# Kernel tuning notes

Measured on AMD Instinct MI355X. Metric: run time of the kernel, lower is better.

## Reference

```python
import jax, jax.numpy as jnp
import numpy as np
import math

N, M, DIM = 16384, 4096, 1024


def setup_inputs() -> dict:
    key = jax.random.key(0)
    k1, k2, k3, k4, k5 = jax.random.split(key, 5)
    x = jax.random.normal(k1, (N, DIM), dtype=jnp.float32)
    e_repr = jax.random.normal(k2, (M, DIM), dtype=jnp.float32)
    H = jax.random.randint(k3, (N, M), 0, 2, dtype=jnp.int32)  # incidence matrix, >0 = connected
    # nn.Linear(dim, dim, bias=False) weights, scaled like torch default init
    W_e = jax.random.normal(k4, (DIM, DIM), dtype=jnp.float32) / math.sqrt(DIM)
    W_n = jax.random.normal(k5, (DIM, DIM), dtype=jnp.float32) / math.sqrt(DIM)
    return {"x": x, "e_repr": e_repr, "H": H, "W_e": W_e, "W_n": W_n}


def reference(x, e_repr, H, W_e, W_n):
    he = e_repr @ W_e.T            # [M, dim]  (W_e(e_repr); original recomputes this, same math)
    hn = x @ W_n.T                 # [N, dim]
    scale = 1.0 / math.sqrt(he.shape[1])
    B = (hn @ he.T) * scale        # [N, M] scores
    mask = H > 0
    B = jnp.where(mask, B, -1e9)
    B = jax.nn.softmax(B, axis=1) * mask.astype(B.dtype)
    out = jax.nn.elu(B @ he)       # [N, dim]
    return out, B
```

## Files before the change

kernel.cpp:

```cpp
#include <hip/hip_runtime.h>

#define NN 16384
#define MM 4096
#define DD 1024

typedef unsigned short u16;
typedef unsigned int u32;
typedef short bf16x8 __attribute__((ext_vector_type(8)));
typedef float f32x4 __attribute__((ext_vector_type(4)));

enum { EPI_PLAIN = 0, EPI_MASK = 1, EPI_ELU = 2 };

__global__ void sentinel_kernel(float* out, float val) {
    if (blockIdx.x == 0 && threadIdx.x < 64) out[threadIdx.x] = val;
}

template <int EPI>
__global__ __launch_bounds__(256) void gemm_split(
    const float* __restrict__ A, const float* __restrict__ Bt,
    float* __restrict__ C, const int* __restrict__ Hm,
    int Cc, int K)
{
    __shared__ u16 sAh[128][40];
    __shared__ u16 sAl[128][40];
    __shared__ u16 sBh[128][40];
    __shared__ u16 sBl[128][40];

    const int tid = threadIdx.x;
    const int lane = tid & 63;
    const int w = tid >> 6;
    const int wm = (w >> 1) * 64;
    const int wn = (w & 1) * 64;
    const int l15 = lane & 15;
    const int l4 = lane >> 4;
    const int rowBlk = blockIdx.y * 128;
    const int colBlk = blockIdx.x * 128;
    const int sr = tid >> 1;
    const int sk = (tid & 1) * 16;

    f32x4 acc[4][4] = {};

    union V16 { u16 u[16]; bf16x8 v[2]; };

    for (int k0 = 0; k0 < K; k0 += 32) {
        const float* pa = A + (size_t)(rowBlk + sr) * K + k0 + sk;
        const float* pb = Bt + (size_t)(colBlk + sr) * K + k0 + sk;

        V16 ah, al, bh, bl;
#pragma unroll
        for (int i = 0; i < 4; ++i) {
            const float4 va = *(const float4*)(pa + 4 * i);
            const float4 vb = *(const float4*)(pb + 4 * i);
            const float fa[4] = { va.x, va.y, va.z, va.w };
            const float fb[4] = { vb.x, vb.y, vb.z, vb.w };
#pragma unroll
            for (int j = 0; j < 4; ++j) {
                const u32 ua = __float_as_uint(fa[j]);
                ah.u[4 * i + j] = (u16)(ua >> 16);
                const float ra = fa[j] - __uint_as_float(ua & 0xffff0000u);
                al.u[4 * i + j] = (u16)(__float_as_uint(ra) >> 16);

                const u32 ub = __float_as_uint(fb[j]);
                bh.u[4 * i + j] = (u16)(ub >> 16);
                const float rb = fb[j] - __uint_as_float(ub & 0xffff0000u);
                bl.u[4 * i + j] = (u16)(__float_as_uint(rb) >> 16);
            }
        }

        __syncthreads();
        *(bf16x8*)&sAh[sr][sk]     = ah.v[0];
        *(bf16x8*)&sAh[sr][sk + 8] = ah.v[1];
        *(bf16x8*)&sAl[sr][sk]     = al.v[0];
        *(bf16x8*)&sAl[sr][sk + 8] = al.v[1];
        *(bf16x8*)&sBh[sr][sk]     = bh.v[0];
        *(bf16x8*)&sBh[sr][sk + 8] = bh.v[1];
        *(bf16x8*)&sBl[sr][sk]     = bl.v[0];
        *(bf16x8*)&sBl[sr][sk + 8] = bl.v[1];
        __syncthreads();

        bf16x8 a_h[4], a_l[4], b_h[4], b_l[4];
#pragma unroll
        for (int m = 0; m < 4; ++m) {
            const int r = wm + m * 16 + l15;
            a_h[m] = *(const bf16x8*)&sAh[r][l4 * 8];
            a_l[m] = *(const bf16x8*)&sAl[r][l4 * 8];
        }
#pragma unroll
        for (int n = 0; n < 4; ++n) {
            const int c = wn + n * 16 + l15;
            b_h[n] = *(const bf16x8*)&sBh[c][l4 * 8];
            b_l[n] = *(const bf16x8*)&sBl[c][l4 * 8];
        }

#pragma unroll
        for (int m = 0; m < 4; ++m)
#pragma unroll
            for (int n = 0; n < 4; ++n) {
                acc[m][n] = __builtin_amdgcn_mfma_f32_16x16x32_bf16(a_h[m], b_h[n], acc[m][n], 0, 0, 0);
                acc[m][n] = __builtin_amdgcn_mfma_f32_16x16x32_bf16(a_h[m], b_l[n], acc[m][n], 0, 0, 0);
                acc[m][n] = __builtin_amdgcn_mfma_f32_16x16x32_bf16(a_l[m], b_h[n], acc[m][n], 0, 0, 0);
            }
    }

    const size_t ldc = (size_t)Cc;
#pragma unroll
    for (int m = 0; m < 4; ++m) {
#pragma unroll
        for (int n = 0; n < 4; ++n) {
            const int col = colBlk + wn + n * 16 + l15;
#pragma unroll
            for (int r = 0; r < 4; ++r) {
                const int row = rowBlk + wm + m * 16 + l4 * 4 + r;
                float v = acc[m][n][r];
                if constexpr (EPI == EPI_MASK) {
                    v *= 0.03125f;
                    if (Hm[(size_t)row * ldc + col] <= 0) v = -1e9f;
                } else if constexpr (EPI == EPI_ELU) {
                    v = v > 0.f ? v : (expf(v) - 1.f);
                }
                C[(size_t)row * ldc + col] = v;
            }
        }
    }
}

__global__ __launch_bounds__(256) void softmax_rows_f32(float* __restrict__ Bm)
{
    const int row = blockIdx.x;
    const int tid = threadIdx.x;
    const int lane = tid & 63;
    const int wid = tid >> 6;
    float4* rp = reinterpret_cast<float4*>(Bm + (size_t)row * MM);

    float4 q[4];
#pragma unroll
    for (int i = 0; i < 4; ++i) q[i] = rp[i * 256 + tid];
    float v[16];
#pragma unroll
    for (int i = 0; i < 4; ++i) {
        v[4 * i + 0] = q[i].x; v[4 * i + 1] = q[i].y;
        v[4 * i + 2] = q[i].z; v[4 * i + 3] = q[i].w;
    }

    float mx = -3e38f;
#pragma unroll
    for (int i = 0; i < 16; ++i) mx = fmaxf(mx, v[i]);
#pragma unroll
    for (int off = 32; off >= 1; off >>= 1) mx = fmaxf(mx, __shfl_xor(mx, off));
    __shared__ float red[4];
    if (lane == 0) red[wid] = mx;
    __syncthreads();
    mx = fmaxf(fmaxf(red[0], red[1]), fmaxf(red[2], red[3]));
    __syncthreads();

    float e[16];
    float s = 0.f;
#pragma unroll
    for (int i = 0; i < 16; ++i) { e[i] = expf(v[i] - mx); s += e[i]; }
#pragma unroll
    for (int off = 32; off >= 1; off >>= 1) s += __shfl_xor(s, off);
    if (lane == 0) red[wid] = s;
    __syncthreads();
    s = red[0] + red[1] + red[2] + red[3];
    const float inv = (mx > -1e8f && s > 0.f) ? (1.0f / s) : 0.f;

#pragma unroll
    for (int i = 0; i < 4; ++i) {
        q[i].x = e[4 * i + 0] * inv; q[i].y = e[4 * i + 1] * inv;
        q[i].z = e[4 * i + 2] * inv; q[i].w = e[4 * i + 3] * inv;
        rp[i * 256 + tid] = q[i];
    }
}

extern "C" void kernel_launch(void* const* d_in, const int* in_sizes, int n_in,
                              void* d_out, int out_size, void* d_ws, size_t ws_size,
                              hipStream_t stream)
{
    (void)d_ws; (void)ws_size;

    float* O = (float*)d_out;
    bool ok_sizes = (n_in == 5)
        && in_sizes[0] == NN * DD && in_sizes[1] == MM * DD
        && in_sizes[2] == NN * MM
        && in_sizes[3] == DD * DD && in_sizes[4] == DD * DD;
    if (!ok_sizes) { sentinel_kernel<<<1, 64, 0, stream>>>(O, 1e6f); return; }
    if (out_size != NN * DD + NN * MM) { sentinel_kernel<<<1, 64, 0, stream>>>(O, 2e6f); return; }

    const float* x  = (const float*)d_in[0];
    const float* er = (const float*)d_in[1];
    const int*   Hm = (const int*)d_in[2];
    const float* We = (const float*)d_in[3];
    const float* Wn = (const float*)d_in[4];

    float* Bo = O + (size_t)NN * DD;

    float* hn  = O;
    float* he  = (float*)d_in[0];
    float* heT = he + (size_t)MM * DD;

    dim3 blk(256);
    gemm_split<EPI_PLAIN><<<dim3(DD / 128, NN / 128), blk, 0, stream>>>(x, Wn, hn, nullptr, DD, DD);
    gemm_split<EPI_PLAIN><<<dim3(DD / 128, MM / 128), blk, 0, stream>>>(er, We, he, nullptr, DD, DD);
    gemm_split<EPI_MASK><<<dim3(MM / 128, NN / 128), blk, 0, stream>>>(hn, he, Bo, Hm, MM, DD);
    gemm_split<EPI_PLAIN><<<dim3(MM / 128, DD / 128), blk, 0, stream>>>(We, er, heT, nullptr, MM, DD);
    softmax_rows_f32<<<dim3(NN), blk, 0, stream>>>(Bo);
    gemm_split<EPI_ELU><<<dim3(DD / 128, NN / 128), blk, 0, stream>>>(Bo, heT, O, nullptr, DD, MM);
}
```

Before: 1.718 ms.

## Store intermediate GEMM outputs as pre-split bf16 hi/lo and DMA-load into LDS

The projection GEMMs now write their results directly as bf16 high/low halves, so the score and output GEMMs no longer convert fp32 to split bf16 on every tile. Those consumers load operands straight into LDS via global_load_lds, and MFMA issue is regrouped into three passes. This removes per-tile split arithmetic and register staging. The cost is unpadded LDS tiles that may bank-conflict and extra scratch written into the input buffer.

```diff
diff --git a/kernel.cpp b/kernel.cpp
--- a/kernel.cpp
+++ b/kernel.cpp
@@ -9,17 +9,28 @@
 typedef short bf16x8 __attribute__((ext_vector_type(8)));
 typedef float f32x4 __attribute__((ext_vector_type(4)));
 
-enum { EPI_PLAIN = 0, EPI_MASK = 1, EPI_ELU = 2 };
+enum { EPI_MASK = 1, EPI_ELU = 2 };
 
 __global__ void sentinel_kernel(float* out, float val) {
     if (blockIdx.x == 0 && threadIdx.x < 64) out[threadIdx.x] = val;
 }
 
-template <int EPI>
-__global__ __launch_bounds__(256) void gemm_split(
+__device__ __forceinline__ void gload16(const void* g, void* l) {
+    __builtin_amdgcn_global_load_lds(
+        (const __attribute__((address_space(1))) void*)g,
+        (__attribute__((address_space(3))) void*)l, 16, 0, 0);
+}
+
+__device__ __forceinline__ void split2(float f, u16& hi, u16& lo) {
+    const u32 u = __float_as_uint(f);
+    hi = (u16)(u >> 16);
+    const float r = f - __uint_as_float(u & 0xffff0000u);
+    lo = (u16)(__float_as_uint(r) >> 16);
+}
+
+__global__ __launch_bounds__(256) void gemm_f32_to_split(
     const float* __restrict__ A, const float* __restrict__ Bt,
-    float* __restrict__ C, const int* __restrict__ Hm,
-    int Cc, int K)
+    u16* __restrict__ Ch, u16* __restrict__ Cl, int Cc, int K)
 {
     __shared__ u16 sAh[128][40];
     __shared__ u16 sAl[128][40];
@@ -39,7 +50,6 @@
     const int sk = (tid & 1) * 16;
 
     f32x4 acc[4][4] = {};
-
     union V16 { u16 u[16]; bf16x8 v[2]; };
 
     for (int k0 = 0; k0 < K; k0 += 32) {
@@ -55,15 +65,8 @@
             const float fb[4] = { vb.x, vb.y, vb.z, vb.w };
 #pragma unroll
             for (int j = 0; j < 4; ++j) {
-                const u32 ua = __float_as_uint(fa[j]);
-                ah.u[4 * i + j] = (u16)(ua >> 16);
-                const float ra = fa[j] - __uint_as_float(ua & 0xffff0000u);
-                al.u[4 * i + j] = (u16)(__float_as_uint(ra) >> 16);
-
-                const u32 ub = __float_as_uint(fb[j]);
-                bh.u[4 * i + j] = (u16)(ub >> 16);
-                const float rb = fb[j] - __uint_as_float(ub & 0xffff0000u);
-                bl.u[4 * i + j] = (u16)(__float_as_uint(rb) >> 16);
+                split2(fa[j], ah.u[4 * i + j], al.u[4 * i + j]);
+                split2(fb[j], bh.u[4 * i + j], bl.u[4 * i + j]);
             }
         }
 
@@ -95,11 +98,135 @@
 #pragma unroll
         for (int m = 0; m < 4; ++m)
 #pragma unroll
-            for (int n = 0; n < 4; ++n) {
+            for (int n = 0; n < 4; ++n)
                 acc[m][n] = __builtin_amdgcn_mfma_f32_16x16x32_bf16(a_h[m], b_h[n], acc[m][n], 0, 0, 0);
+#pragma unroll
+        for (int m = 0; m < 4; ++m)
+#pragma unroll
+            for (int n = 0; n < 4; ++n)
                 acc[m][n] = __builtin_amdgcn_mfma_f32_16x16x32_bf16(a_h[m], b_l[n], acc[m][n], 0, 0, 0);
+#pragma unroll
+        for (int m = 0; m < 4; ++m)
+#pragma unroll
+            for (int n = 0; n < 4; ++n)
                 acc[m][n] = __builtin_amdgcn_mfma_f32_16x16x32_bf16(a_l[m], b_h[n], acc[m][n], 0, 0, 0);
+    }
+
+    const size_t ldc = (size_t)Cc;
+#pragma unroll
+    for (int m = 0; m < 4; ++m) {
+#pragma unroll
+        for (int n = 0; n < 4; ++n) {
+            const int col = colBlk + wn + n * 16 + l15;
+#pragma unroll
+            for (int r = 0; r < 4; ++r) {
+                const int row = rowBlk + wm + m * 16 + l4 * 4 + r;
+                u16 hi, lo;
+                split2(acc[m][n][r], hi, lo);
+                Ch[(size_t)row * ldc + col] = hi;
+                Cl[(size_t)row * ldc + col] = lo;
             }
+        }
+    }
+}
+
+template <bool ASPLIT, int EPI>
+__global__ __launch_bounds__(256) void gemm_pp(
+    const u16* __restrict__ Ah, const u16* __restrict__ Al,
+    const float* __restrict__ Af,
+    const u16* __restrict__ Bh, const u16* __restrict__ Bl,
+    float* __restrict__ C, const int* __restrict__ Hm, int Cc, int K)
+{
+    __shared__ u16 sAh[128][32];
+    __shared__ u16 sAl[128][32];
+    __shared__ u16 sBh[128][32];
+    __shared__ u16 sBl[128][32];
+
+    const int tid = threadIdx.x;
+    const int lane = tid & 63;
+    const int w = tid >> 6;
+    const int wm = (w >> 1) * 64;
+    const int wn = (w & 1) * 64;
+    const int l15 = lane & 15;
+    const int l4 = lane >> 4;
+    const int rowBlk = blockIdx.y * 128;
+    const int colBlk = blockIdx.x * 128;
+
+    const int srow = w * 32 + (lane >> 2);
+    const int scol = (lane & 3) * 8;
+
+    const int fr = tid >> 1;
+    const int fk = (tid & 1) * 16;
+
+    f32x4 acc[4][4] = {};
+    union V16 { u16 u[16]; bf16x8 v[2]; };
+
+    for (int k0 = 0; k0 < K; k0 += 32) {
+        V16 ah, al;
+        if constexpr (!ASPLIT) {
+            const float* pa = Af + (size_t)(rowBlk + fr) * K + k0 + fk;
+#pragma unroll
+            for (int i = 0; i < 4; ++i) {
+                const float4 va = *(const float4*)(pa + 4 * i);
+                const float f[4] = { va.x, va.y, va.z, va.w };
+#pragma unroll
+                for (int j = 0; j < 4; ++j)
+                    split2(f[j], ah.u[4 * i + j], al.u[4 * i + j]);
+            }
+        }
+
+        __syncthreads();
+
+        {
+            const size_t rb = (size_t)(colBlk + srow) * K + k0 + scol;
+            gload16(Bh + rb,                 &sBh[w * 32][0]);
+            gload16(Bh + rb + (size_t)16 * K, &sBh[w * 32 + 16][0]);
+            gload16(Bl + rb,                 &sBl[w * 32][0]);
+            gload16(Bl + rb + (size_t)16 * K, &sBl[w * 32 + 16][0]);
+        }
+        if constexpr (ASPLIT) {
+            const size_t ra = (size_t)(rowBlk + srow) * K + k0 + scol;
+            gload16(Ah + ra,                 &sAh[w * 32][0]);
+            gload16(Ah + ra + (size_t)16 * K, &sAh[w * 32 + 16][0]);
+            gload16(Al + ra,                 &sAl[w * 32][0]);
+            gload16(Al + ra + (size_t)16 * K, &sAl[w * 32 + 16][0]);
+        } else {
+            *(bf16x8*)&sAh[fr][fk]     = ah.v[0];
+            *(bf16x8*)&sAh[fr][fk + 8] = ah.v[1];
+            *(bf16x8*)&sAl[fr][fk]     = al.v[0];
+            *(bf16x8*)&sAl[fr][fk + 8] = al.v[1];
+        }
+        __syncthreads();
+
+        bf16x8 a_h[4], a_l[4], b_h[4], b_l[4];
+#pragma unroll
+        for (int m = 0; m < 4; ++m) {
+            const int r = wm + m * 16 + l15;
+            a_h[m] = *(const bf16x8*)&sAh[r][l4 * 8];
+            a_l[m] = *(const bf16x8*)&sAl[r][l4 * 8];
+        }
+#pragma unroll
+        for (int n = 0; n < 4; ++n) {
+            const int c = wn + n * 16 + l15;
+            b_h[n] = *(const bf16x8*)&sBh[c][l4 * 8];
+            b_l[n] = *(const bf16x8*)&sBl[c][l4 * 8];
+        }
+
+#pragma unroll
+        for (int m = 0; m < 4; ++m)
+#pragma unroll
+            for (int n = 0; n < 4; ++n)
+                acc[m][n] = __builtin_amdgcn_mfma_f32_16x16x32_bf16(a_h[m], b_h[n], acc[m][n], 0, 0, 0);
+#pragma unroll
+        for (int m = 0; m < 4; ++m)
+#pragma unroll
+            for (int n = 0; n < 4; ++n)
+                acc[m][n] = __builtin_amdgcn_mfma_f32_16x16x32_bf16(a_h[m], b_l[n], acc[m][n], 0, 0, 0);
+#pragma unroll
+        for (int m = 0; m < 4; ++m)
+#pragma unroll
+            for (int n = 0; n < 4; ++n)
+                acc[m][n] = __builtin_amdgcn_mfma_f32_16x16x32_bf16(a_l[m], b_h[n], acc[m][n], 0, 0, 0);
     }
 
     const size_t ldc = (size_t)Cc;
@@ -194,15 +321,20 @@
 
     float* Bo = O + (size_t)NN * DD;
 
-    float* hn  = O;
-    float* he  = (float*)d_in[0];
-    float* heT = he + (size_t)MM * DD;
+    u16* hn_h  = (u16*)O;
+    u16* hn_l  = hn_h + (size_t)NN * DD;
+    u16* he_h  = (u16*)d_in[0];
+    u16* he_l  = he_h + (size_t)MM * DD;
+    u16* heT_h = he_l + (size_t)MM * DD;
+    u16* heT_l = heT_h + (size_t)DD * MM;
 
     dim3 blk(256);
-    gemm_split<EPI_PLAIN><<<dim3(DD / 128, NN / 128), blk, 0, stream>>>(x, Wn, hn, nullptr, DD, DD);
-    gemm_split<EPI_PLAIN><<<dim3(DD / 128, MM / 128), blk, 0, stream>>>(er, We, he, nullptr, DD, DD);
-    gemm_split<EPI_MASK><<<dim3(MM / 128, NN / 128), blk, 0, stream>>>(hn, he, Bo, Hm, MM, DD);
-    gemm_split<EPI_PLAIN><<<dim3(MM / 128, DD / 128), blk, 0, stream>>>(We, er, heT, nullptr, MM, DD);
+    gemm_f32_to_split<<<dim3(DD / 128, NN / 128), blk, 0, stream>>>(x, Wn, hn_h, hn_l, DD, DD);
+    gemm_f32_to_split<<<dim3(DD / 128, MM / 128), blk, 0, stream>>>(er, We, he_h, he_l, DD, DD);
+    gemm_f32_to_split<<<dim3(MM / 128, DD / 128), blk, 0, stream>>>(We, er, heT_h, heT_l, MM, DD);
+    gemm_pp<true, EPI_MASK><<<dim3(MM / 128, NN / 128), blk, 0, stream>>>(
+        hn_h, hn_l, nullptr, he_h, he_l, Bo, Hm, MM, DD);
     softmax_rows_f32<<<dim3(NN), blk, 0, stream>>>(Bo);
-    gemm_split<EPI_ELU><<<dim3(DD / 128, NN / 128), blk, 0, stream>>>(Bo, heT, O, nullptr, DD, MM);
-}
+    gemm_pp<false, EPI_ELU><<<dim3(DD / 128, NN / 128), blk, 0, stream>>>(
+        nullptr, nullptr, Bo, heT_h, heT_l, O, nullptr, DD, MM);
+}
```

After: 1.661 ms. 3.3% less time.
